# Optimization experiments

Measured on AMD Instinct MI355X. Metric: run time of the kernel, lower is better.

## Reference

```python
import jax, jax.numpy as jnp
import numpy as np

W = 8          # window_size (small/key side)
WU = 2 * W     # window_size_up (big/query side)
H = 4          # num_heads
SF = 128       # sf_dim
BF = 256       # bf_dim
HD = SF // H   # head_dim = 32
SCALE = HD ** -0.5
TABLE = (2 * WU - 1) * (2 * W - 1)  # 465


def _relative_position_index():
    # big coords (2, WU*WU), small coords (2, W*W), 'ij' meshgrid like torch
    ch, cw = jnp.meshgrid(jnp.arange(WU), jnp.arange(WU), indexing='ij')
    big = jnp.stack([ch.reshape(-1), cw.reshape(-1)])          # (2, Nb)
    sh, sw = jnp.meshgrid(jnp.arange(W), jnp.arange(W), indexing='ij')
    small = jnp.stack([sh.reshape(-1), sw.reshape(-1)])        # (2, Ns)
    rel = big[:, :, None] - small[:, None, :]                  # (2, Nb, Ns)
    idx = (rel[0] + W - 1) * (2 * W - 1) + (rel[1] + W - 1)    # (Nb, Ns)
    return idx


def setup_inputs() -> dict:
    key = jax.random.key(0)
    ks = jax.random.split(key, 9)
    B_ = 1024
    Nb, Ns = WU * WU, W * W
    inp = {
        'big_x': jax.random.normal(ks[0], (B_, Nb, BF), jnp.float32),
        'small_x': jax.random.normal(ks[1], (B_, Ns, SF), jnp.float32),
        # proj1: bf_dim -> sf_dim
        'W1': jax.random.normal(ks[2], (BF, SF), jnp.float32) * (BF ** -0.5),
        'b1': jnp.zeros((SF,), jnp.float32),
        # fused qkv: sf_dim -> 3*sf_dim
        'Wqkv': jax.random.normal(ks[3], (SF, 3 * SF), jnp.float32) * (SF ** -0.5),
        'bqkv': jnp.zeros((3 * SF,), jnp.float32),
        # proj2: sf_dim -> bf_dim
        'W2': jax.random.normal(ks[4], (SF, BF), jnp.float32) * (SF ** -0.5),
        'b2': jnp.zeros((BF,), jnp.float32),
        # relative position bias table, trunc_normal std=0.02
        'bias_table': jax.random.normal(ks[5], (TABLE, H), jnp.float32) * 0.02,
    }
    return inp


def reference(big_x, small_x, W1, b1, Wqkv, bqkv, W2, b2, bias_table):
    B_, Nb, _ = big_x.shape
    Ns = small_x.shape[1]

    big = big_x @ W1 + b1                                      # (B, Nb, SF)

    # only q of big and k,v of small are used downstream
    qb = (big @ Wqkv[:, :SF] + bqkv[:SF]).reshape(B_, Nb, H, HD)
    ks_ = (small_x @ Wqkv[:, SF:2 * SF] + bqkv[SF:2 * SF]).reshape(B_, Ns, H, HD)
    vs = (small_x @ Wqkv[:, 2 * SF:] + bqkv[2 * SF:]).reshape(B_, Ns, H, HD)

    attn = jnp.einsum('bqhd,bkhd->bhqk', qb * SCALE, ks_)      # (B, H, Nb, Ns)

    idx = _relative_position_index()                           # (Nb, Ns)
    bias = bias_table[idx]                                     # (Nb, Ns, H)
    attn = attn + jnp.transpose(bias, (2, 0, 1))[None]         # broadcast over B

    attn = jax.nn.softmax(attn, axis=-1)
    out = jnp.einsum('bhqk,bkhd->bqhd', attn, vs).reshape(B_, Nb, SF)
    return out @ W2 + b2                                       # (B, Nb, BF)
```

## Files before the change

kernel.cpp:

```cpp
#include <hip/hip_runtime.h>
#include <stdint.h>

#define NH      4
#define SF      128
#define BF      256
#define HD      32
#define NB      256
#define NS      64
#define NBATCH  1024

typedef short bf16x8 __attribute__((ext_vector_type(8)));
typedef float f32x4  __attribute__((ext_vector_type(4)));

#define WEFFT_OFF 0
#define BEFF_OFF  65536
#define WKVT_OFF  66048
#define W2T_OFF   131584
#define BMATT_OFF 197120

#define LDS_SK  0
#define LDS_SVT 16384
#define LDS_SQ  32768
#define LDS_STG 65536
#define LDS_TOTAL 81920

__device__ __forceinline__ short f2b(float x){
  uint32_t u = __float_as_uint(x);
  u += 0x7fff + ((u >> 16) & 1);
  return (short)(u >> 16);
}
__device__ __forceinline__ uint32_t cvt_pk_bf16(float lo, float hi){
  uint32_t r;
  asm("v_cvt_pk_bf16_f32 %0, %1, %2" : "=v"(r) : "v"(lo), "v"(hi));
  return r;
}
__device__ __forceinline__ int swz256(int row, int byteInRow){
  return row * 256 + (byteInRow ^ ((row & 7) << 4));
}
__device__ __forceinline__ int swz128(int row, int byteInRow){
  return row * 128 + (byteInRow ^ ((row & 7) << 4));
}

__global__ void cowin_prep(const float* __restrict__ W1, const float* __restrict__ b1,
                           const float* __restrict__ Wqkv, const float* __restrict__ bqkv,
                           const float* __restrict__ W2, const float* __restrict__ tbl,
                           void* ws)
{
  short* weffT = (short*)((char*)ws + WEFFT_OFF);
  float* beff  = (float*)((char*)ws + BEFF_OFF);
  short* wkvT  = (short*)((char*)ws + WKVT_OFF);
  short* w2T   = (short*)((char*)ws + W2T_OFF);
  float* bmatT = (float*)((char*)ws + BMATT_OFF);
  const float L2E = 1.4426950408889634f;
  const float QS  = 0.17677669529663687f * L2E;

  int bid = blockIdx.x, t = threadIdx.x;
  if (bid < 128){
    int n = bid, k = t;
    float acc = 0.f;
    for (int c = 0; c < SF; ++c) acc += W1[k * SF + c] * Wqkv[c * (3*SF) + n];
    weffT[n * 256 + k] = f2b(acc * QS);
  } else if (bid == 128){
    if (t < 128){
      int n = t;
      float acc = bqkv[n];
      for (int c = 0; c < SF; ++c) acc += b1[c] * Wqkv[c * (3*SF) + n];
      beff[n] = acc * QS;
    }
  } else if (bid < 145){
    int base = (bid - 129) * 2048 + t * 8;
    for (int j = 0; j < 8; ++j){
      int i = base + j, n = i >> 7, k = i & 127;
      wkvT[i] = f2b(Wqkv[k * (3*SF) + SF + n]);
    }
  } else if (bid < 161){
    int base = (bid - 145) * 2048 + t * 8;
    for (int j = 0; j < 8; ++j){
      int i = base + j, n = i >> 7, k = i & 127;
      w2T[i] = f2b(W2[k * BF + n]);
    }
  } else {
    int i = (bid - 161) * 256 + t;
    int h = i >> 14, kk = (i >> 8) & 63, q = i & 255;
    int qh = q >> 4, qw = q & 15, kh = kk >> 3, kw = kk & 7;
    int idx = (qh - kh + 7) * 15 + (qw - kw + 7);
    bmatT[i] = tbl[idx * 4 + h] * L2E;
  }
}

__global__ __launch_bounds__(256, 2) void cowin_main(
    const float* __restrict__ big_x, const float* __restrict__ small_x,
    const float* __restrict__ bqkv,  const float* __restrict__ b2,
    const void* __restrict__ ws, float* __restrict__ out)
{
  extern __shared__ char smem[];
  const short* weffT = (const short*)((const char*)ws + WEFFT_OFF);
  const float* beff  = (const float*)((const char*)ws + BEFF_OFF);
  const short* wkvT  = (const short*)((const char*)ws + WKVT_OFF);
  const short* w2T   = (const short*)((const char*)ws + W2T_OFF);
  const float* bmatT = (const float*)((const char*)ws + BMATT_OFF);

  const int bid = blockIdx.x;
  const int b  = bid >> 1;
  const int hf = bid & 1;
  const int t    = threadIdx.x;
  const int w    = t >> 6;
  const int lane = t & 63;
  const int li   = lane & 15;
  const int g    = lane >> 4;

  const f32x4 vzero = {0.f, 0.f, 0.f, 0.f};

  {
    const float* sx = small_x + (size_t)b * (NS * SF);
    int tok = t >> 2, q4 = t & 3;
    const float4* src = (const float4*)(sx + tok * SF + q4 * 32);
    float4 v[8];
    #pragma unroll
    for (int j = 0; j < 8; ++j) v[j] = src[j];
    uint32_t pk[16];
    #pragma unroll
    for (int j = 0; j < 8; ++j){
      pk[2*j]   = cvt_pk_bf16(v[j].x, v[j].y);
      pk[2*j+1] = cvt_pk_bf16(v[j].z, v[j].w);
    }
    #pragma unroll
    for (int c = 0; c < 4; ++c){
      uint4 u; u.x = pk[c*4]; u.y = pk[c*4+1]; u.z = pk[c*4+2]; u.w = pk[c*4+3];
      *(uint4*)(smem + LDS_SK + swz256(tok, q4 * 64 + c * 16)) = u;
    }
  }
  __syncthreads();

  f32x4 kv[4][4];
  #pragma unroll
  for (int m = 0; m < 4; ++m)
    #pragma unroll
    for (int n = 0; n < 4; ++n) kv[m][n] = vzero;

  #pragma unroll
  for (int ks = 0; ks < 4; ++ks){
    bf16x8 afr[4];
    #pragma unroll
    for (int m = 0; m < 4; ++m)
      afr[m] = *(const bf16x8*)(smem + LDS_SK + swz256(m*16 + li, (ks*32 + g*8) * 2));
    #pragma unroll
    for (int n4 = 0; n4 < 4; ++n4){
      int n = w * 64 + n4 * 16 + li;
      bf16x8 bfr = *(const bf16x8*)(wkvT + n * 128 + ks * 32 + g * 8);
      #pragma unroll
      for (int m = 0; m < 4; ++m)
        kv[m][n4] = __builtin_amdgcn_mfma_f32_16x16x32_bf16(afr[m], bfr, kv[m][n4], 0, 0, 0);
    }
  }
  __syncthreads();

  if (w < 2){
    #pragma unroll
    for (int n4 = 0; n4 < 4; ++n4){
      int feat = w * 64 + n4 * 16 + li;
      float bias = bqkv[SF + feat];
      #pragma unroll
      for (int m = 0; m < 4; ++m){
        f32x4 vv = kv[m][n4];
        uint32_t p0 = cvt_pk_bf16(vv[0] + bias, vv[1] + bias);
        uint32_t p1 = cvt_pk_bf16(vv[2] + bias, vv[3] + bias);
        int tok0 = m * 16 + g * 4;
        *(short*)(smem + LDS_SK + swz256(tok0 + 0, feat * 2)) = (short)(p0);
        *(short*)(smem + LDS_SK + swz256(tok0 + 1, feat * 2)) = (short)(p0 >> 16);
        *(short*)(smem + LDS_SK + swz256(tok0 + 2, feat * 2)) = (short)(p1);
        *(short*)(smem + LDS_SK + swz256(tok0 + 3, feat * 2)) = (short)(p1 >> 16);
      }
    }
  } else {
    #pragma unroll
    for (int n4 = 0; n4 < 4; ++n4){
      int feat = (w - 2) * 64 + n4 * 16 + li;
      float bias = bqkv[2 * SF + feat];
      #pragma unroll
      for (int m = 0; m < 4; ++m){
        f32x4 vv = kv[m][n4];
        uint2 u;
        u.x = cvt_pk_bf16(vv[0] + bias, vv[1] + bias);
        u.y = cvt_pk_bf16(vv[2] + bias, vv[3] + bias);
        *(uint2*)(smem + LDS_SVT + swz128(feat, (m * 16 + g * 4) * 2)) = u;
      }
    }
  }
  __syncthreads();

  f32x4 qacc[8][2];
  #pragma unroll
  for (int m = 0; m < 8; ++m){ qacc[m][0] = vzero; qacc[m][1] = vzero; }

  const float* bx = big_x + (size_t)b * NB * BF + (size_t)hf * 128 * BF;
  const int qrow = t >> 1, qh32 = (t & 1) * 32;

  float4 ld[8];
  {
    const float4* s_ = (const float4*)(bx + qrow * BF + qh32);
    #pragma unroll
    for (int j = 0; j < 8; ++j) ld[j] = s_[j];
  }
  for (int kc = 0; kc < 4; ++kc){
    uint32_t pk[16];
    #pragma unroll
    for (int j = 0; j < 8; ++j){
      pk[2*j]   = cvt_pk_bf16(ld[j].x, ld[j].y);
      pk[2*j+1] = cvt_pk_bf16(ld[j].z, ld[j].w);
    }
    __syncthreads();
    #pragma unroll
    for (int c = 0; c < 4; ++c){
      uint4 u; u.x = pk[c*4]; u.y = pk[c*4+1]; u.z = pk[c*4+2]; u.w = pk[c*4+3];
      *(uint4*)(smem + LDS_STG + swz128(qrow, qh32 * 2 + c * 16)) = u;
    }
    __syncthreads();
    if (kc < 3){
      const float4* s_ = (const float4*)(bx + qrow * BF + (kc + 1) * 64 + qh32);
      #pragma unroll
      for (int j = 0; j < 8; ++j) ld[j] = s_[j];
    }
    #pragma unroll
    for (int ks = 0; ks < 2; ++ks){
      bf16x8 afr[8];
      #pragma unroll
      for (int m = 0; m < 8; ++m)
        afr[m] = *(const bf16x8*)(smem + LDS_STG + swz128(m*16 + li, (ks*32 + g*8) * 2));
      #pragma unroll
      for (int nt = 0; nt < 2; ++nt){
        int n = w * 32 + nt * 16 + li;
        bf16x8 bfr = *(const bf16x8*)(weffT + n * 256 + kc * 64 + ks * 32 + g * 8);
        #pragma unroll
        for (int m = 0; m < 8; ++m)
          qacc[m][nt] = __builtin_amdgcn_mfma_f32_16x16x32_bf16(afr[m], bfr, qacc[m][nt], 0, 0, 0);
      }
    }
  }

  #pragma unroll
  for (int nt = 0; nt < 2; ++nt){
    int feat = w * 32 + nt * 16 + li;
    float be = beff[feat];
    #pragma unroll
    for (int m = 0; m < 8; ++m){
      f32x4 vv = qacc[m][nt];
      uint32_t p0 = cvt_pk_bf16(vv[0] + be, vv[1] + be);
      uint32_t p1 = cvt_pk_bf16(vv[2] + be, vv[3] + be);
      int r0 = m * 16 + g * 4;
      *(short*)(smem + LDS_SQ + swz256(r0 + 0, feat * 2)) = (short)(p0);
      *(short*)(smem + LDS_SQ + swz256(r0 + 1, feat * 2)) = (short)(p0 >> 16);
      *(short*)(smem + LDS_SQ + swz256(r0 + 2, feat * 2)) = (short)(p1);
      *(short*)(smem + LDS_SQ + swz256(r0 + 3, feat * 2)) = (short)(p1 >> 16);
    }
  }
  __syncthreads();

  f32x4 sacc[4][8];
  #pragma unroll
  for (int m = 0; m < 4; ++m)
    #pragma unroll
    for (int n = 0; n < 8; ++n) sacc[m][n] = vzero;
  {
    bf16x8 afr[4];
    #pragma unroll
    for (int m = 0; m < 4; ++m)
      afr[m] = *(const bf16x8*)(smem + LDS_SK + swz256(m*16 + li, (w*32 + g*8) * 2));
    #pragma unroll
    for (int n = 0; n < 8; ++n){
      bf16x8 bfr = *(const bf16x8*)(smem + LDS_SQ + swz256(n*16 + li, (w*32 + g*8) * 2));
      #pragma unroll
      for (int m = 0; m < 4; ++m)
        sacc[m][n] = __builtin_amdgcn_mfma_f32_16x16x32_bf16(afr[m], bfr, sacc[m][n], 0, 0, 0);
    }
  }
  __syncthreads();

  {
    const float* bm = bmatT + w * (64 * 256);
    #pragma unroll
    for (int m = 0; m < 4; ++m){
      #pragma unroll
      for (int n = 0; n < 8; ++n){
        int qg = hf * 128 + n * 16 + li;
        #pragma unroll
        for (int r = 0; r < 4; ++r){
          int key = m * 16 + g * 4 + r;
          sacc[m][n][r] += bm[key * 256 + qg];
        }
      }
    }
  }

  float sm[8];
  #pragma unroll
  for (int n = 0; n < 8; ++n){
    float mx = sacc[0][n][0];
    #pragma unroll
    for (int m = 0; m < 4; ++m)
      #pragma unroll
      for (int r = 0; r < 4; ++r) mx = fmaxf(mx, sacc[m][n][r]);
    mx = fmaxf(mx, __shfl_xor(mx, 16));
    mx = fmaxf(mx, __shfl_xor(mx, 32));
    float s0 = 0.f;
    #pragma unroll
    for (int m = 0; m < 4; ++m)
      #pragma unroll
      for (int r = 0; r < 4; ++r){
        float e = __builtin_amdgcn_exp2f(sacc[m][n][r] - mx);
        sacc[m][n][r] = e;
        s0 += e;
      }
    s0 += __shfl_xor(s0, 16);
    s0 += __shfl_xor(s0, 32);
    sm[n] = __builtin_amdgcn_rcpf(s0);
  }

  f32x4 oacc[2][2][4];
  #pragma unroll
  for (int hl = 0; hl < 2; ++hl)
    #pragma unroll
    for (int m2 = 0; m2 < 2; ++m2)
      #pragma unroll
      for (int n4 = 0; n4 < 4; ++n4) oacc[hl][m2][n4] = vzero;

  char* sp = smem + LDS_SQ + w * 8192;
  #pragma unroll
  for (int hl = 0; hl < 2; ++hl){
    #pragma unroll
    for (int n4 = 0; n4 < 4; ++n4){
      int n = hl * 4 + n4;
      #pragma unroll
      for (int m = 0; m < 4; ++m){
        uint2 u;
        u.x = cvt_pk_bf16(sacc[m][n][0], sacc[m][n][1]);
        u.y = cvt_pk_bf16(sacc[m][n][2], sacc[m][n][3]);
        *(uint2*)(sp + swz128(n4 * 16 + li, (m * 16 + g * 4) * 2)) = u;
      }
    }
    #pragma unroll
    for (int kk = 0; kk < 2; ++kk){
      bf16x8 afr[2];
      #pragma unroll
      for (int m2 = 0; m2 < 2; ++m2)
        afr[m2] = *(const bf16x8*)(smem + LDS_SVT + swz128(w*32 + m2*16 + li, (kk*32 + g*8) * 2));
      #pragma unroll
      for (int n4 = 0; n4 < 4; ++n4){
        bf16x8 bfr = *(const bf16x8*)(sp + swz128(n4 * 16 + li, (kk*32 + g*8) * 2));
        #pragma unroll
        for (int m2 = 0; m2 < 2; ++m2)
          oacc[hl][m2][n4] = __builtin_amdgcn_mfma_f32_16x16x32_bf16(afr[m2], bfr, oacc[hl][m2][n4], 0, 0, 0);
      }
    }
  }
  __syncthreads();

  #pragma unroll
  for (int hl = 0; hl < 2; ++hl)
    #pragma unroll
    for (int m2 = 0; m2 < 2; ++m2)
      #pragma unroll
      for (int n4 = 0; n4 < 4; ++n4){
        float rs = sm[hl * 4 + n4];
        f32x4 vv = oacc[hl][m2][n4];
        uint2 u;
        u.x = cvt_pk_bf16(vv[0] * rs, vv[1] * rs);
        u.y = cvt_pk_bf16(vv[2] * rs, vv[3] * rs);
        *(uint2*)(smem + swz256(hl*64 + n4*16 + li, (w*32 + m2*16 + g*4) * 2)) = u;
      }
  __syncthreads();

  f32x4 facc[8][4];
  #pragma unroll
  for (int m = 0; m < 8; ++m)
    #pragma unroll
    for (int nt = 0; nt < 4; ++nt) facc[m][nt] = vzero;

  #pragma unroll
  for (int kc = 0; kc < 4; ++kc){
    bf16x8 afr[8];
    #pragma unroll
    for (int m = 0; m < 8; ++m)
      afr[m] = *(const bf16x8*)(smem + swz256(m*16 + li, (kc*32 + g*8) * 2));
    #pragma unroll
    for (int nt = 0; nt < 4; ++nt){
      int n = w * 64 + nt * 16 + li;
      bf16x8 bfr = *(const bf16x8*)(w2T + n * 128 + kc * 32 + g * 8);
      #pragma unroll
      for (int m = 0; m < 8; ++m)
        facc[m][nt] = __builtin_amdgcn_mfma_f32_16x16x32_bf16(afr[m], bfr, facc[m][nt], 0, 0, 0);
    }
  }

  float* op = out + (size_t)b * NB * BF + (size_t)hf * 128 * BF;
  #pragma unroll
  for (int nt = 0; nt < 4; ++nt){
    int col = w * 64 + nt * 16 + li;
    float bb = b2[col];
    #pragma unroll
    for (int m = 0; m < 8; ++m){
      int r0 = m * 16 + g * 4;
      #pragma unroll
      for (int r = 0; r < 4; ++r)
        op[(size_t)(r0 + r) * BF + col] = facc[m][nt][r] + bb;
    }
  }
}

extern "C" void kernel_launch(void* const* d_in, const int* in_sizes, int n_in,
                              void* d_out, int out_size, void* d_ws, size_t ws_size,
                              hipStream_t stream)
{
  const float* big_x   = (const float*)d_in[0];
  const float* small_x = (const float*)d_in[1];
  const float* W1      = (const float*)d_in[2];
  const float* b1      = (const float*)d_in[3];
  const float* Wqkv    = (const float*)d_in[4];
  const float* bqkv    = (const float*)d_in[5];
  const float* W2      = (const float*)d_in[6];
  const float* b2      = (const float*)d_in[7];
  const float* tbl     = (const float*)d_in[8];
  float* out = (float*)d_out;

  (void)in_sizes; (void)n_in; (void)out_size; (void)ws_size;

  cowin_prep<<<417, 256, 0, stream>>>(W1, b1, Wqkv, bqkv, W2, tbl, d_ws);

  hipFuncSetAttribute(reinterpret_cast<const void*>(cowin_main),
                      hipFuncAttributeMaxDynamicSharedMemorySize, LDS_TOTAL);
  cowin_main<<<NBATCH * 2, 256, LDS_TOTAL, stream>>>(big_x, small_x, bqkv, b2, d_ws, out);
}
```

Before: 189.5 us.

## Use 512-thread blocks, double-buffer big_x staging, and cut LDS to 64KB

Doubles the threads per block from 256 to 512 and re-partitions every GEMM stage and the attention stage across 8 waves, giving each wave half the columns or queries. The big_x staging buffer is folded into the Q region as a double buffer, which removes one barrier per k-chunk and lets the first big_x load overlap the KV projection. LDS per block drops from 80KB to 64KB, aiming for more resident waves and better latency hiding. In exchange, each wave does less work per barrier, and the relative-position bias gather is split across more waves.

```diff
diff --git a/kernel.cpp b/kernel.cpp
--- a/kernel.cpp
+++ b/kernel.cpp
@@ -21,8 +21,7 @@
 #define LDS_SK  0
 #define LDS_SVT 16384
 #define LDS_SQ  32768
-#define LDS_STG 65536
-#define LDS_TOTAL 81920
+#define LDS_TOTAL 65536
 
 __device__ __forceinline__ short f2b(float x){
   uint32_t u = __float_as_uint(x);
@@ -88,7 +87,7 @@
   }
 }
 
-__global__ __launch_bounds__(256, 2) void cowin_main(
+__global__ __launch_bounds__(512, 4) void cowin_main(
     const float* __restrict__ big_x, const float* __restrict__ small_x,
     const float* __restrict__ bqkv,  const float* __restrict__ b2,
     const void* __restrict__ ws, float* __restrict__ out)
@@ -111,32 +110,39 @@
 
   const f32x4 vzero = {0.f, 0.f, 0.f, 0.f};
 
+  const float* bx = big_x + (size_t)b * NB * BF + (size_t)hf * 128 * BF;
+  const int qrow = t >> 2, qq = (t & 3) * 16;
+
+  float4 ld[4];
   {
     const float* sx = small_x + (size_t)b * (NS * SF);
-    int tok = t >> 2, q4 = t & 3;
-    const float4* src = (const float4*)(sx + tok * SF + q4 * 32);
-    float4 v[8];
-    #pragma unroll
-    for (int j = 0; j < 8; ++j) v[j] = src[j];
-    uint32_t pk[16];
-    #pragma unroll
-    for (int j = 0; j < 8; ++j){
-      pk[2*j]   = cvt_pk_bf16(v[j].x, v[j].y);
-      pk[2*j+1] = cvt_pk_bf16(v[j].z, v[j].w);
-    }
-    #pragma unroll
-    for (int c = 0; c < 4; ++c){
+    int tok = t >> 3, p = t & 7;
+    const float4* src = (const float4*)(sx + tok * SF + p * 16);
+    float4 sv[4];
+    #pragma unroll
+    for (int j = 0; j < 4; ++j) sv[j] = src[j];
+    {
+      const float4* s_ = (const float4*)(bx + qrow * BF + qq);
+      #pragma unroll
+      for (int j = 0; j < 4; ++j) ld[j] = s_[j];
+    }
+    uint32_t pk[8];
+    #pragma unroll
+    for (int j = 0; j < 4; ++j){
+      pk[2*j]   = cvt_pk_bf16(sv[j].x, sv[j].y);
+      pk[2*j+1] = cvt_pk_bf16(sv[j].z, sv[j].w);
+    }
+    #pragma unroll
+    for (int c = 0; c < 2; ++c){
       uint4 u; u.x = pk[c*4]; u.y = pk[c*4+1]; u.z = pk[c*4+2]; u.w = pk[c*4+3];
-      *(uint4*)(smem + LDS_SK + swz256(tok, q4 * 64 + c * 16)) = u;
-    }
-  }
-  __syncthreads();
-
-  f32x4 kv[4][4];
-  #pragma unroll
-  for (int m = 0; m < 4; ++m)
-    #pragma unroll
-    for (int n = 0; n < 4; ++n) kv[m][n] = vzero;
+      *(uint4*)(smem + LDS_SK + swz256(tok, p * 32 + c * 16)) = u;
+    }
+  }
+  __syncthreads();
+
+  f32x4 kv[4][2];
+  #pragma unroll
+  for (int m = 0; m < 4; ++m){ kv[m][0] = vzero; kv[m][1] = vzero; }
 
   #pragma unroll
   for (int ks = 0; ks < 4; ++ks){
@@ -145,24 +151,24 @@
     for (int m = 0; m < 4; ++m)
       afr[m] = *(const bf16x8*)(smem + LDS_SK + swz256(m*16 + li, (ks*32 + g*8) * 2));
     #pragma unroll
-    for (int n4 = 0; n4 < 4; ++n4){
-      int n = w * 64 + n4 * 16 + li;
+    for (int n2 = 0; n2 < 2; ++n2){
+      int n = w * 32 + n2 * 16 + li;
       bf16x8 bfr = *(const bf16x8*)(wkvT + n * 128 + ks * 32 + g * 8);
       #pragma unroll
       for (int m = 0; m < 4; ++m)
-        kv[m][n4] = __builtin_amdgcn_mfma_f32_16x16x32_bf16(afr[m], bfr, kv[m][n4], 0, 0, 0);
-    }
-  }
-  __syncthreads();
-
-  if (w < 2){
-    #pragma unroll
-    for (int n4 = 0; n4 < 4; ++n4){
-      int feat = w * 64 + n4 * 16 + li;
+        kv[m][n2] = __builtin_amdgcn_mfma_f32_16x16x32_bf16(afr[m], bfr, kv[m][n2], 0, 0, 0);
+    }
+  }
+  __syncthreads();
+
+  if (w < 4){
+    #pragma unroll
+    for (int n2 = 0; n2 < 2; ++n2){
+      int feat = w * 32 + n2 * 16 + li;
       float bias = bqkv[SF + feat];
       #pragma unroll
       for (int m = 0; m < 4; ++m){
-        f32x4 vv = kv[m][n4];
+        f32x4 vv = kv[m][n2];
         uint32_t p0 = cvt_pk_bf16(vv[0] + bias, vv[1] + bias);
         uint32_t p1 = cvt_pk_bf16(vv[2] + bias, vv[3] + bias);
         int tok0 = m * 16 + g * 4;
@@ -174,12 +180,12 @@
     }
   } else {
     #pragma unroll
-    for (int n4 = 0; n4 < 4; ++n4){
-      int feat = (w - 2) * 64 + n4 * 16 + li;
+    for (int n2 = 0; n2 < 2; ++n2){
+      int feat = (w - 4) * 32 + n2 * 16 + li;
       float bias = bqkv[2 * SF + feat];
       #pragma unroll
       for (int m = 0; m < 4; ++m){
-        f32x4 vv = kv[m][n4];
+        f32x4 vv = kv[m][n2];
         uint2 u;
         u.x = cvt_pk_bf16(vv[0] + bias, vv[1] + bias);
         u.y = cvt_pk_bf16(vv[2] + bias, vv[3] + bias);
@@ -187,64 +193,72 @@
       }
     }
   }
-  __syncthreads();
-
-  f32x4 qacc[8][2];
-  #pragma unroll
-  for (int m = 0; m < 8; ++m){ qacc[m][0] = vzero; qacc[m][1] = vzero; }
-
-  const float* bx = big_x + (size_t)b * NB * BF + (size_t)hf * 128 * BF;
-  const int qrow = t >> 1, qh32 = (t & 1) * 32;
-
-  float4 ld[8];
+
+  f32x4 qacc[8];
+  #pragma unroll
+  for (int m = 0; m < 8; ++m) qacc[m] = vzero;
+
   {
-    const float4* s_ = (const float4*)(bx + qrow * BF + qh32);
-    #pragma unroll
-    for (int j = 0; j < 8; ++j) ld[j] = s_[j];
-  }
-  for (int kc = 0; kc < 4; ++kc){
-    uint32_t pk[16];
-    #pragma unroll
-    for (int j = 0; j < 8; ++j){
+    uint32_t pk[8];
+    #pragma unroll
+    for (int j = 0; j < 4; ++j){
       pk[2*j]   = cvt_pk_bf16(ld[j].x, ld[j].y);
       pk[2*j+1] = cvt_pk_bf16(ld[j].z, ld[j].w);
     }
-    __syncthreads();
-    #pragma unroll
-    for (int c = 0; c < 4; ++c){
+    char* buf0 = smem + LDS_SQ;
+    #pragma unroll
+    for (int c = 0; c < 2; ++c){
       uint4 u; u.x = pk[c*4]; u.y = pk[c*4+1]; u.z = pk[c*4+2]; u.w = pk[c*4+3];
-      *(uint4*)(smem + LDS_STG + swz128(qrow, qh32 * 2 + c * 16)) = u;
-    }
+      *(uint4*)(buf0 + swz128(qrow, qq * 2 + c * 16)) = u;
+    }
+    const float4* s_ = (const float4*)(bx + qrow * BF + 64 + qq);
+    #pragma unroll
+    for (int j = 0; j < 4; ++j) ld[j] = s_[j];
+  }
+
+  for (int kc = 0; kc < 4; ++kc){
     __syncthreads();
     if (kc < 3){
-      const float4* s_ = (const float4*)(bx + qrow * BF + (kc + 1) * 64 + qh32);
-      #pragma unroll
-      for (int j = 0; j < 8; ++j) ld[j] = s_[j];
-    }
+      uint32_t pk[8];
+      #pragma unroll
+      for (int j = 0; j < 4; ++j){
+        pk[2*j]   = cvt_pk_bf16(ld[j].x, ld[j].y);
+        pk[2*j+1] = cvt_pk_bf16(ld[j].z, ld[j].w);
+      }
+      char* bufn = smem + LDS_SQ + ((kc + 1) & 1) * 16384;
+      #pragma unroll
+      for (int c = 0; c < 2; ++c){
+        uint4 u; u.x = pk[c*4]; u.y = pk[c*4+1]; u.z = pk[c*4+2]; u.w = pk[c*4+3];
+        *(uint4*)(bufn + swz128(qrow, qq * 2 + c * 16)) = u;
+      }
+      if (kc < 2){
+        const float4* s_ = (const float4*)(bx + qrow * BF + (kc + 2) * 64 + qq);
+        #pragma unroll
+        for (int j = 0; j < 4; ++j) ld[j] = s_[j];
+      }
+    }
+    const char* buf = smem + LDS_SQ + (kc & 1) * 16384;
+    const int n = w * 16 + li;
     #pragma unroll
     for (int ks = 0; ks < 2; ++ks){
       bf16x8 afr[8];
       #pragma unroll
       for (int m = 0; m < 8; ++m)
-        afr[m] = *(const bf16x8*)(smem + LDS_STG + swz128(m*16 + li, (ks*32 + g*8) * 2));
-      #pragma unroll
-      for (int nt = 0; nt < 2; ++nt){
-        int n = w * 32 + nt * 16 + li;
-        bf16x8 bfr = *(const bf16x8*)(weffT + n * 256 + kc * 64 + ks * 32 + g * 8);
-        #pragma unroll
-        for (int m = 0; m < 8; ++m)
-          qacc[m][nt] = __builtin_amdgcn_mfma_f32_16x16x32_bf16(afr[m], bfr, qacc[m][nt], 0, 0, 0);
-      }
-    }
-  }
-
-  #pragma unroll
-  for (int nt = 0; nt < 2; ++nt){
-    int feat = w * 32 + nt * 16 + li;
+        afr[m] = *(const bf16x8*)(buf + swz128(m*16 + li, (ks*32 + g*8) * 2));
+      bf16x8 bfr = *(const bf16x8*)(weffT + n * 256 + kc * 64 + ks * 32 + g * 8);
+      #pragma unroll
+      for (int m = 0; m < 8; ++m)
+        qacc[m] = __builtin_amdgcn_mfma_f32_16x16x32_bf16(afr[m], bfr, qacc[m], 0, 0, 0);
+    }
+  }
+  __syncthreads();
+
+  {
+    int feat = w * 16 + li;
     float be = beff[feat];
     #pragma unroll
     for (int m = 0; m < 8; ++m){
-      f32x4 vv = qacc[m][nt];
+      f32x4 vv = qacc[m];
       uint32_t p0 = cvt_pk_bf16(vv[0] + be, vv[1] + be);
       uint32_t p1 = cvt_pk_bf16(vv[2] + be, vv[3] + be);
       int r0 = m * 16 + g * 4;
@@ -256,19 +270,21 @@
   }
   __syncthreads();
 
-  f32x4 sacc[4][8];
+  const int h  = w & 3;
+  const int qh = w >> 2;
+  f32x4 sacc[4][4];
   #pragma unroll
   for (int m = 0; m < 4; ++m)
     #pragma unroll
-    for (int n = 0; n < 8; ++n) sacc[m][n] = vzero;
+    for (int n = 0; n < 4; ++n) sacc[m][n] = vzero;
   {
     bf16x8 afr[4];
     #pragma unroll
     for (int m = 0; m < 4; ++m)
-      afr[m] = *(const bf16x8*)(smem + LDS_SK + swz256(m*16 + li, (w*32 + g*8) * 2));
-    #pragma unroll
-    for (int n = 0; n < 8; ++n){
-      bf16x8 bfr = *(const bf16x8*)(smem + LDS_SQ + swz256(n*16 + li, (w*32 + g*8) * 2));
+      afr[m] = *(const bf16x8*)(smem + LDS_SK + swz256(m*16 + li, (h*32 + g*8) * 2));
+    #pragma unroll
+    for (int n = 0; n < 4; ++n){
+      bf16x8 bfr = *(const bf16x8*)(smem + LDS_SQ + swz256(qh*64 + n*16 + li, (h*32 + g*8) * 2));
       #pragma unroll
       for (int m = 0; m < 4; ++m)
         sacc[m][n] = __builtin_amdgcn_mfma_f32_16x16x32_bf16(afr[m], bfr, sacc[m][n], 0, 0, 0);
@@ -277,12 +293,12 @@
   __syncthreads();
 
   {
-    const float* bm = bmatT + w * (64 * 256);
+    const float* bm = bmatT + h * (64 * 256);
     #pragma unroll
     for (int m = 0; m < 4; ++m){
       #pragma unroll
-      for (int n = 0; n < 8; ++n){
-        int qg = hf * 128 + n * 16 + li;
+      for (int n = 0; n < 4; ++n){
+        int qg = hf * 128 + qh * 64 + n * 16 + li;
         #pragma unroll
         for (int r = 0; r < 4; ++r){
           int key = m * 16 + g * 4 + r;
@@ -292,9 +308,9 @@
     }
   }
 
-  float sm[8];
-  #pragma unroll
-  for (int n = 0; n < 8; ++n){
+  float sm[4];
+  #pragma unroll
+  for (int n = 0; n < 4; ++n){
     float mx = sacc[0][n][0];
     #pragma unroll
     for (int m = 0; m < 4; ++m)
@@ -316,20 +332,20 @@
     sm[n] = __builtin_amdgcn_rcpf(s0);
   }
 
-  f32x4 oacc[2][2][4];
+  f32x4 oacc[2][2][2];
   #pragma unroll
   for (int hl = 0; hl < 2; ++hl)
     #pragma unroll
     for (int m2 = 0; m2 < 2; ++m2)
       #pragma unroll
-      for (int n4 = 0; n4 < 4; ++n4) oacc[hl][m2][n4] = vzero;
-
-  char* sp = smem + LDS_SQ + w * 8192;
+      for (int n4 = 0; n4 < 2; ++n4) oacc[hl][m2][n4] = vzero;
+
+  char* sp = smem + LDS_SQ + w * 4096;
   #pragma unroll
   for (int hl = 0; hl < 2; ++hl){
     #pragma unroll
-    for (int n4 = 0; n4 < 4; ++n4){
-      int n = hl * 4 + n4;
+    for (int n4 = 0; n4 < 2; ++n4){
+      int n = hl * 2 + n4;
       #pragma unroll
       for (int m = 0; m < 4; ++m){
         uint2 u;
@@ -343,9 +359,9 @@
       bf16x8 afr[2];
       #pragma unroll
       for (int m2 = 0; m2 < 2; ++m2)
-        afr[m2] = *(const bf16x8*)(smem + LDS_SVT + swz128(w*32 + m2*16 + li, (kk*32 + g*8) * 2));
-      #pragma unroll
-      for (int n4 = 0; n4 < 4; ++n4){
+        afr[m2] = *(const bf16x8*)(smem + LDS_SVT + swz128(h*32 + m2*16 + li, (kk*32 + g*8) * 2));
+      #pragma unroll
+      for (int n4 = 0; n4 < 2; ++n4){
         bf16x8 bfr = *(const bf16x8*)(sp + swz128(n4 * 16 + li, (kk*32 + g*8) * 2));
         #pragma unroll
         for (int m2 = 0; m2 < 2; ++m2)
@@ -360,21 +376,20 @@
     #pragma unroll
     for (int m2 = 0; m2 < 2; ++m2)
       #pragma unroll
-      for (int n4 = 0; n4 < 4; ++n4){
-        float rs = sm[hl * 4 + n4];
+      for (int n4 = 0; n4 < 2; ++n4){
+        float rs = sm[hl * 2 + n4];
         f32x4 vv = oacc[hl][m2][n4];
         uint2 u;
         u.x = cvt_pk_bf16(vv[0] * rs, vv[1] * rs);
         u.y = cvt_pk_bf16(vv[2] * rs, vv[3] * rs);
-        *(uint2*)(smem + swz256(hl*64 + n4*16 + li, (w*32 + m2*16 + g*4) * 2)) = u;
-      }
-  __syncthreads();
-
-  f32x4 facc[8][4];
-  #pragma unroll
-  for (int m = 0; m < 8; ++m)
-    #pragma unroll
-    for (int nt = 0; nt < 4; ++nt) facc[m][nt] = vzero;
+        int q = qh * 64 + hl * 32 + n4 * 16 + li;
+        *(uint2*)(smem + swz256(q, (h*32 + m2*16 + g*4) * 2)) = u;
+      }
+  __syncthreads();
+
+  f32x4 facc[8][2];
+  #pragma unroll
+  for (int m = 0; m < 8; ++m){ facc[m][0] = vzero; facc[m][1] = vzero; }
 
   #pragma unroll
   for (int kc = 0; kc < 4; ++kc){
@@ -383,8 +398,8 @@
     for (int m = 0; m < 8; ++m)
       afr[m] = *(const bf16x8*)(smem + swz256(m*16 + li, (kc*32 + g*8) * 2));
     #pragma unroll
-    for (int nt = 0; nt < 4; ++nt){
-      int n = w * 64 + nt * 16 + li;
+    for (int nt = 0; nt < 2; ++nt){
+      int n = w * 32 + nt * 16 + li;
       bf16x8 bfr = *(const bf16x8*)(w2T + n * 128 + kc * 32 + g * 8);
       #pragma unroll
       for (int m = 0; m < 8; ++m)
@@ -394,8 +409,8 @@
 
   float* op = out + (size_t)b * NB * BF + (size_t)hf * 128 * BF;
   #pragma unroll
-  for (int nt = 0; nt < 4; ++nt){
-    int col = w * 64 + nt * 16 + li;
+  for (int nt = 0; nt < 2; ++nt){
+    int col = w * 32 + nt * 16 + li;
     float bb = b2[col];
     #pragma unroll
     for (int m = 0; m < 8; ++m){
@@ -428,5 +443,5 @@
 
   hipFuncSetAttribute(reinterpret_cast<const void*>(cowin_main),
                       hipFuncAttributeMaxDynamicSharedMemorySize, LDS_TOTAL);
-  cowin_main<<<NBATCH * 2, 256, LDS_TOTAL, stream>>>(big_x, small_x, bqkv, b2, d_ws, out);
-}
+  cowin_main<<<NBATCH * 2, 512, LDS_TOTAL, stream>>>(big_x, small_x, bqkv, b2, d_ws, out);
+}
```

Measured after the change: 179.3 us. 5.3% less time.
